# Kernel tuning notes

Hardware: AMD Instinct MI355X
Metric: run time of the kernel (lower is better)

The kernel has to match this reference:

```python
import jax, jax.numpy as jnp
import numpy as np

L, S, N, E, H = 2048, 2048, 4, 1024, 16
D = E // H  # head_dim = 64


def setup_inputs() -> dict:
    key = jax.random.key(0)
    ks = jax.random.split(key, 7)
    scale = 1.0 / np.sqrt(E)
    return {
        "query": jax.random.normal(ks[0], (L, N, E), jnp.float32),
        "key": jax.random.normal(ks[1], (S, N, E), jnp.float32),
        "value": jax.random.normal(ks[2], (S, N, E), jnp.float32),
        "in_proj_w": jax.random.normal(ks[3], (3 * E, E), jnp.float32) * scale,
        "in_proj_b": jax.random.normal(ks[4], (3 * E,), jnp.float32) * 0.01,
        "out_proj_w": jax.random.normal(ks[5], (E, E), jnp.float32) * scale * 0.25,
        "out_proj_b": jax.random.normal(ks[6], (E,), jnp.float32) * 0.01,
    }


def reference(query, key, value, in_proj_w, in_proj_b, out_proj_w, out_proj_b):
    # Split packed in-projection into q/k/v parts (torch layout: [3E, E]).
    wq, wk, wv = in_proj_w[:E], in_proj_w[E:2 * E], in_proj_w[2 * E:]
    bq, bk, bv = in_proj_b[:E], in_proj_b[E:2 * E], in_proj_b[2 * E:]

    def proj(x, w, b):  # (T,N,E) -> (N,H,T,D)
        y = jnp.einsum('tne,fe->tnf', x, w) + b
        T = x.shape[0]
        return y.reshape(T, N, H, D).transpose(1, 2, 0, 3)

    q = proj(query, wq, bq) * (1.0 / np.sqrt(D))  # scale queries
    k = proj(key, wk, bk)
    v = proj(value, wv, bv)

    scores = jnp.einsum('nhld,nhsd->nhls', q, k)  # (N,H,L,S)
    attn = jax.nn.softmax(scores, axis=-1)
    ctx = jnp.einsum('nhls,nhsd->nhld', attn, v)  # (N,H,L,D)
    ctx = ctx.transpose(2, 0, 1, 3).reshape(L, N, E)  # (L,N,E)

    out = jnp.einsum('lne,fe->lnf', ctx, out_proj_w) + out_proj_b
    attn_weights = attn.mean(axis=1)  # (N,L,S), averaged over heads (torch default)
    return out, attn_weights
```

## Files before the change

kernel.cpp:

```cpp
#include <hip/hip_runtime.h>
#include <hip/hip_bf16.h>

#define L_ 2048
#define S_ 2048
#define NB 4
#define E_ 1024
#define H_ 16
#define D_ 64
#define LDT 72
#define NCH (S_ / 64)

typedef __attribute__((ext_vector_type(8))) short bf16x8;
typedef __attribute__((ext_vector_type(4))) float f32x4;

__device__ __forceinline__ short f2bf(float f) {
  union { float f; unsigned u; } v; v.f = f;
  unsigned r = v.u + 0x7FFFu + ((v.u >> 16) & 1u);
  return (short)(r >> 16);
}
__device__ __forceinline__ float bf2f(short s) {
  union { unsigned u; float f; } v; v.u = ((unsigned)(unsigned short)s) << 16;
  return v.f;
}
__device__ __forceinline__ unsigned cvt_pk_bf16(float lo, float hi) {
  unsigned r;
  asm("v_cvt_pk_bf16_f32 %0, %1, %2" : "=v"(r) : "v"(lo), "v"(hi));
  return r;
}

#define LGKM_BARRIER() do {                                   \
    asm volatile("s_waitcnt lgkmcnt(0)" ::: "memory");        \
    __builtin_amdgcn_sched_barrier(0);                        \
    __builtin_amdgcn_s_barrier();                             \
    __builtin_amdgcn_sched_barrier(0);                        \
  } while (0)

__global__ void k_convert(const float* __restrict__ wi, const float* __restrict__ wo,
                          short* __restrict__ wqkv, short* __restrict__ wout) {
  const int n1 = 3 * E_ * E_ / 4;
  const int n2 = E_ * E_ / 4;
  const int stride = gridDim.x * blockDim.x;
  for (int i = blockIdx.x * blockDim.x + threadIdx.x; i < n1 + n2; i += stride) {
    const float4* s; short* d; int j;
    if (i < n1) { s = (const float4*)wi; d = wqkv; j = i; }
    else        { s = (const float4*)wo; d = wout; j = i - n1; }
    float4 v = s[j];
    uint2 o; o.x = cvt_pk_bf16(v.x, v.y); o.y = cvt_pk_bf16(v.z, v.w);
    *(uint2*)&d[(size_t)j * 4] = o;
  }
}

__global__ __launch_bounds__(256) void k_qkv(
    const float* __restrict__ qin, const float* __restrict__ kin, const float* __restrict__ vin,
    const short* __restrict__ wbf, const float* __restrict__ bias,
    short* __restrict__ qh, short* __restrict__ kh, short* __restrict__ vh) {
  __shared__ short As[128 * LDT];
  __shared__ short Bs[128 * LDT];
  const int bm = blockIdx.x;
  const int fbase = blockIdx.y * 128;
  const int mat = fbase >> 10;
  const float* __restrict__ A = (mat == 0) ? qin : (mat == 1) ? kin : vin;
  short* __restrict__ dst = (mat == 0) ? qh : (mat == 1) ? kh : vh;
  const float scale = (mat == 0) ? 0.125f * 1.44269504088896f : 1.0f;
  const int tid = threadIdx.x;
  const int lane = tid & 63, wid = tid >> 6;
  const int wr = wid >> 1, wc = wid & 1;
  const int lr = lane & 15, lk = lane >> 4;
  f32x4 acc[4][4] = {};

  for (int kb = 0; kb < E_; kb += 64) {
#pragma unroll
    for (int i = 0; i < 8; ++i) {
      int f4 = i * 256 + tid;
      int row = f4 >> 4, k4 = f4 & 15;
      float4 v = *(const float4*)&A[(size_t)(bm * 128 + row) * E_ + kb + k4 * 4];
      uint2 o; o.x = cvt_pk_bf16(v.x, v.y); o.y = cvt_pk_bf16(v.z, v.w);
      *(uint2*)&As[row * LDT + k4 * 4] = o;
    }
#pragma unroll
    for (int i = 0; i < 4; ++i) {
      int e8 = i * 256 + tid;
      int row = e8 >> 3, k8 = e8 & 7;
      int4 v = *(const int4*)&wbf[(size_t)(fbase + row) * E_ + kb + k8 * 8];
      *(int4*)&Bs[row * LDT + k8 * 8] = v;
    }
    __syncthreads();
#pragma unroll
    for (int kk = 0; kk < 2; ++kk) {
      bf16x8 a[4], b[4];
#pragma unroll
      for (int fi = 0; fi < 4; ++fi)
        a[fi] = *(const bf16x8*)&As[(wr * 64 + fi * 16 + lr) * LDT + kk * 32 + lk * 8];
#pragma unroll
      for (int ci = 0; ci < 4; ++ci)
        b[ci] = *(const bf16x8*)&Bs[(wc * 64 + ci * 16 + lr) * LDT + kk * 32 + lk * 8];
#pragma unroll
      for (int fi = 0; fi < 4; ++fi)
#pragma unroll
        for (int ci = 0; ci < 4; ++ci)
          acc[fi][ci] = __builtin_amdgcn_mfma_f32_16x16x32_bf16(a[fi], b[ci], acc[fi][ci], 0, 0, 0);
    }
    __syncthreads();
  }
#pragma unroll
  for (int ci = 0; ci < 4; ++ci) {
    const int fg = fbase + wc * 64 + ci * 16 + lr;
    const float b = bias[fg];
    const int col = fg & 1023;
    const int h = col >> 6, d = col & 63;
#pragma unroll
    for (int fi = 0; fi < 4; ++fi)
#pragma unroll
      for (int j = 0; j < 4; ++j) {
        int m = bm * 128 + wr * 64 + fi * 16 + lk * 4 + j;
        int t = m >> 2, n = m & 3;
        float vv = (acc[fi][ci][j] + b) * scale;
        dst[(((size_t)(n * H_ + h) * L_ + t) << 6) + d] = f2bf(vv);
      }
  }
}

__global__ __launch_bounds__(256) void k_vtrans(const short* __restrict__ vh,
                                                short* __restrict__ vt) {
  __shared__ short t[64][LDT];
  const int nh = blockIdx.y;
  const int tb = blockIdx.x;
  const int tid = threadIdx.x;
  const short* __restrict__ src = vh + ((size_t)nh * L_ + tb * 64) * D_;
  short* __restrict__ dst = vt + (size_t)nh * S_ * D_;
#pragma unroll
  for (int i = 0; i < 2; ++i) {
    int v = i * 256 + tid;
    int r = v >> 3, c8 = v & 7;
    *(bf16x8*)&t[r][c8 * 8] = *(const bf16x8*)&src[(size_t)r * D_ + c8 * 8];
  }
  __syncthreads();
#pragma unroll
  for (int i = 0; i < 2; ++i) {
    int v = i * 256 + tid;
    int d = v >> 3, t8 = v & 7;
    bf16x8 o;
#pragma unroll
    for (int e = 0; e < 8; ++e) o[e] = t[t8 * 8 + e][d];
    int sb = tb * 2 + (t8 >> 2);
    *(bf16x8*)&dst[(size_t)sb * (D_ * 32) + d * 32 + (t8 & 3) * 8] = o;
  }
}

__global__ __launch_bounds__(256) void k_stats(
    const short* __restrict__ qh, const short* __restrict__ kh, float* __restrict__ rl) {
  const int nh = blockIdx.y;
  const int qt = blockIdx.x;
  const short* __restrict__ Q = qh + (size_t)nh * L_ * D_;
  const short* __restrict__ K = kh + (size_t)nh * S_ * D_;
  const int tid = threadIdx.x;
  const int lane = tid & 63, wid = tid >> 6;
  const int lr = lane & 15, lk = lane >> 4;
  const int rbase = qt * 128 + wid * 32;
  bf16x8 a[2][2];
#pragma unroll
  for (int ri = 0; ri < 2; ++ri)
#pragma unroll
    for (int kk = 0; kk < 2; ++kk)
      a[ri][kk] = *(const bf16x8*)&Q[(size_t)(rbase + ri * 16 + lr) * D_ + kk * 32 + lk * 8];
  bf16x8 kst[4][2];
#pragma unroll
  for (int ci = 0; ci < 4; ++ci) {
    kst[ci][0] = *(const bf16x8*)&K[(size_t)(ci * 16 + lr) * D_ + lk * 8];
    kst[ci][1] = *(const bf16x8*)&K[(size_t)(ci * 16 + lr) * D_ + 32 + lk * 8];
  }
  float ssum[2][4] = {};
  for (int st = 0; st < S_; st += 64) {
    const int stn = (st + 64 < S_) ? st + 64 : st;
    f32x4 acc[2][4] = {};
#pragma unroll
    for (int ci = 0; ci < 4; ++ci) {
#pragma unroll
      for (int ri = 0; ri < 2; ++ri) {
        acc[ri][ci] = __builtin_amdgcn_mfma_f32_16x16x32_bf16(a[ri][0], kst[ci][0], acc[ri][ci], 0, 0, 0);
        acc[ri][ci] = __builtin_amdgcn_mfma_f32_16x16x32_bf16(a[ri][1], kst[ci][1], acc[ri][ci], 0, 0, 0);
      }
      kst[ci][0] = *(const bf16x8*)&K[(size_t)(stn + ci * 16 + lr) * D_ + lk * 8];
      kst[ci][1] = *(const bf16x8*)&K[(size_t)(stn + ci * 16 + lr) * D_ + 32 + lk * 8];
    }
#pragma unroll
    for (int ri = 0; ri < 2; ++ri)
#pragma unroll
      for (int j = 0; j < 4; ++j) {
        float s = __builtin_amdgcn_exp2f(acc[ri][0][j]) + __builtin_amdgcn_exp2f(acc[ri][1][j]) +
                  __builtin_amdgcn_exp2f(acc[ri][2][j]) + __builtin_amdgcn_exp2f(acc[ri][3][j]);
        s += __shfl_xor(s, 1);
        s += __shfl_xor(s, 2);
        s += __shfl_xor(s, 4);
        s += __shfl_xor(s, 8);
        ssum[ri][j] += s;
      }
  }
  if (lr == 0) {
#pragma unroll
    for (int ri = 0; ri < 2; ++ri)
#pragma unroll
      for (int j = 0; j < 4; ++j)
        rl[(size_t)nh * L_ + rbase + ri * 16 + lk * 4 + j] = 1.0f / ssum[ri][j];
  }
}

__global__ __launch_bounds__(1024) void k_attn(
    const short* __restrict__ qh, const short* __restrict__ kh, const short* __restrict__ vt,
    const float* __restrict__ rl, float* __restrict__ attnw, short* __restrict__ ctx) {
  extern __shared__ char psl[];
  const int bid = blockIdx.x;
  const int xcd = bid & 7;
  const int n = xcd >> 1;
  const int qt = (bid >> 3) | ((xcd & 1) << 5);
  const int tid = threadIdx.x;
  const int h = tid >> 6, lane = tid & 63;
  const int lr = lane & 15, lk = lane >> 4;
  const int rbase = qt * 32;
  const size_t nh = (size_t)(n * H_ + h);
  const short* __restrict__ K = kh + nh * S_ * D_;
  const short* __restrict__ VT = vt + nh * S_ * D_;
  char* const slab0 = psl + h * 4096;

  bf16x8 qf[2][2];
  float rls[2];
  {
    const short* Q = qh + nh * L_ * D_;
#pragma unroll
    for (int li = 0; li < 2; ++li) {
#pragma unroll
      for (int kk = 0; kk < 2; ++kk)
        qf[li][kk] = *(const bf16x8*)&Q[(size_t)(rbase + li * 16 + lr) * D_ + kk * 32 + lk * 8];
      rls[li] = rl[nh * L_ + rbase + li * 16 + lr];
    }
  }
  f32x4 cacc[2][4] = {};
  const int mrow = tid >> 5, mc2 = (tid & 31) * 2;
  float* awp = attnw + ((size_t)n * L_ + rbase + mrow) * S_ + mc2;
  const int moff = mrow * 128 + ((mc2 * 2) ^ ((mrow & 7) << 4));

  for (int ch = 0; ch < NCH; ++ch) {
    const int st = ch * 64;
    char* const sl = slab0 + (ch & 1) * 65536;
    bf16x8 kf[4][2];
#pragma unroll
    for (int u = 0; u < 4; ++u) {
      kf[u][0] = *(const bf16x8*)&K[(size_t)(st + u * 16 + lr) * D_ + lk * 8];
      kf[u][1] = *(const bf16x8*)&K[(size_t)(st + u * 16 + lr) * D_ + 32 + lk * 8];
    }
    bf16x8 vb[4][2];
#pragma unroll
    for (int b = 0; b < 2; ++b) {
      const size_t sb = (size_t)((st >> 5) + b) * (D_ * 32);
#pragma unroll
      for (int ci = 0; ci < 4; ++ci)
        vb[ci][b] = *(const bf16x8*)&VT[sb + (ci * 16 + lr) * 32 + lk * 8];
    }
#pragma unroll
    for (int u = 0; u < 4; ++u) {
#pragma unroll
      for (int li = 0; li < 2; ++li) {
        f32x4 sc = {};
        sc = __builtin_amdgcn_mfma_f32_16x16x32_bf16(kf[u][0], qf[li][0], sc, 0, 0, 0);
        sc = __builtin_amdgcn_mfma_f32_16x16x32_bf16(kf[u][1], qf[li][1], sc, 0, 0, 0);
        uint2 pk;
        pk.x = cvt_pk_bf16(__builtin_amdgcn_exp2f(sc[0]) * rls[li],
                           __builtin_amdgcn_exp2f(sc[1]) * rls[li]);
        pk.y = cvt_pk_bf16(__builtin_amdgcn_exp2f(sc[2]) * rls[li],
                           __builtin_amdgcn_exp2f(sc[3]) * rls[li]);
        const int row = li * 16 + lr;
        *(uint2*)(sl + row * 128 + ((u * 32 + lk * 8) ^ ((row & 7) << 4))) = pk;
      }
    }
#pragma unroll
    for (int b = 0; b < 2; ++b)
#pragma unroll
      for (int li = 0; li < 2; ++li) {
        const int row = li * 16 + lr;
        bf16x8 pa = *(const bf16x8*)(sl + row * 128 + ((b * 64 + lk * 16) ^ ((row & 7) << 4)));
#pragma unroll
        for (int ci = 0; ci < 4; ++ci)
          cacc[li][ci] = __builtin_amdgcn_mfma_f32_16x16x32_bf16(pa, vb[ci][b], cacc[li][ci], 0, 0, 0);
      }
    if (ch > 0) {
      char* const ms = psl + (((ch & 1) ^ 1)) * 65536;
      float s0 = 0.f, s1 = 0.f;
#pragma unroll
      for (int hh = 0; hh < 16; ++hh) {
        short2 m = *(const short2*)(ms + hh * 4096 + moff);
        s0 += bf2f(m.x); s1 += bf2f(m.y);
      }
      *(float2*)&awp[st - 64] = make_float2(s0 * 0.0625f, s1 * 0.0625f);
    }
    LGKM_BARRIER();
  }
  {
    char* const ms = psl + 65536;
    float s0 = 0.f, s1 = 0.f;
#pragma unroll
    for (int hh = 0; hh < 16; ++hh) {
      short2 m = *(const short2*)(ms + hh * 4096 + moff);
      s0 += bf2f(m.x); s1 += bf2f(m.y);
    }
    *(float2*)&awp[S_ - 64] = make_float2(s0 * 0.0625f, s1 * 0.0625f);
  }
#pragma unroll
  for (int li = 0; li < 2; ++li)
#pragma unroll
    for (int ci = 0; ci < 4; ++ci)
#pragma unroll
      for (int j = 0; j < 4; ++j) {
        int row = rbase + li * 16 + lk * 4 + j;
        int d = ci * 16 + lr;
        ctx[((size_t)row * NB + n) * E_ + h * 64 + d] = f2bf(cacc[li][ci][j]);
      }
}

__global__ __launch_bounds__(256) void k_out(
    const short* __restrict__ ctxb, const short* __restrict__ wbf,
    const float* __restrict__ bias, float* __restrict__ out) {
  __shared__ short As[128 * LDT];
  __shared__ short Bs[128 * LDT];
  const int bm = blockIdx.x, bn = blockIdx.y;
  const int tid = threadIdx.x;
  const int lane = tid & 63, wid = tid >> 6;
  const int wr = wid >> 1, wc = wid & 1;
  const int lr = lane & 15, lk = lane >> 4;
  f32x4 acc[4][4] = {};
  for (int kb = 0; kb < E_; kb += 64) {
#pragma unroll
    for (int i = 0; i < 4; ++i) {
      int e8 = i * 256 + tid;
      int row = e8 >> 3, k8 = e8 & 7;
      int4 va = *(const int4*)&ctxb[(size_t)(bm * 128 + row) * E_ + kb + k8 * 8];
      *(int4*)&As[row * LDT + k8 * 8] = va;
      int4 vb = *(const int4*)&wbf[(size_t)(bn * 128 + row) * E_ + kb + k8 * 8];
      *(int4*)&Bs[row * LDT + k8 * 8] = vb;
    }
    __syncthreads();
#pragma unroll
    for (int kk = 0; kk < 2; ++kk) {
      bf16x8 a[4], b[4];
#pragma unroll
      for (int fi = 0; fi < 4; ++fi)
        a[fi] = *(const bf16x8*)&As[(wr * 64 + fi * 16 + lr) * LDT + kk * 32 + lk * 8];
#pragma unroll
      for (int ci = 0; ci < 4; ++ci)
        b[ci] = *(const bf16x8*)&Bs[(wc * 64 + ci * 16 + lr) * LDT + kk * 32 + lk * 8];
#pragma unroll
      for (int fi = 0; fi < 4; ++fi)
#pragma unroll
        for (int ci = 0; ci < 4; ++ci)
          acc[fi][ci] = __builtin_amdgcn_mfma_f32_16x16x32_bf16(a[fi], b[ci], acc[fi][ci], 0, 0, 0);
    }
    __syncthreads();
  }
#pragma unroll
  for (int ci = 0; ci < 4; ++ci) {
    int col = bn * 128 + wc * 64 + ci * 16 + lr;
    float b = bias[col];
#pragma unroll
    for (int fi = 0; fi < 4; ++fi)
#pragma unroll
      for (int j = 0; j < 4; ++j) {
        int m = bm * 128 + wr * 64 + fi * 16 + lk * 4 + j;
        out[(size_t)m * E_ + col] = acc[fi][ci][j] + b;
      }
  }
}

extern "C" void kernel_launch(void* const* d_in, const int* in_sizes, int n_in,
                              void* d_out, int out_size, void* d_ws, size_t ws_size,
                              hipStream_t stream) {
  const float* qin = (const float*)d_in[0];
  const float* kin = (const float*)d_in[1];
  const float* vin = (const float*)d_in[2];
  const float* wi  = (const float*)d_in[3];
  const float* bi  = (const float*)d_in[4];
  const float* wo  = (const float*)d_in[5];
  const float* bo  = (const float*)d_in[6];
  float* out = (float*)d_out;
  float* attnw = out + (size_t)L_ * NB * E_;

  short* wqkv = (short*)d_ws;
  short* wout = wqkv + (size_t)3 * E_ * E_;
  short* qh = wout + (size_t)E_ * E_;
  short* kh = qh + (size_t)NB * L_ * E_;
  short* vh = kh + (size_t)NB * L_ * E_;
  short* vt = vh + (size_t)NB * L_ * E_;
  float* rl = (float*)(vt + (size_t)NB * L_ * E_);
  short* ctx = (short*)(rl + (size_t)NB * H_ * L_);

  k_convert<<<1024, 256, 0, stream>>>(wi, wo, wqkv, wout);
  k_qkv<<<dim3(64, 24), 256, 0, stream>>>(qin, kin, vin, wqkv, bi, qh, kh, vh);
  k_vtrans<<<dim3(32, 64), 256, 0, stream>>>(vh, vt);
  k_stats<<<dim3(16, 64), 256, 0, stream>>>(qh, kh, rl);
  k_attn<<<256, 1024, 131072, stream>>>(qh, kh, vt, rl, attnw, ctx);
  k_out<<<dim3(64, 8), 256, 0, stream>>>(ctx, wout, bo, out);
}
```

Baseline: 453.0 us.

## Split attention over key halves, fuse V transpose into QKV projection

The attention kernel now launches twice as many blocks, and each block handles half of the key chunks. The two partial context results go to separate buffers and are summed in the out-projection load. Shared memory drops to a single 64KB slab, so the double buffering is gone and an extra barrier is added per chunk, which aims for more resident blocks and better CU fill. The separate V-transpose kernel is removed and the QKV projection writes V straight into the transposed layout with scattered 2-byte stores. The partial contexts are rounded to bf16 before they are summed, which adds rounding error, and the ctx traffic doubles.

```diff
diff --git a/kernel.cpp b/kernel.cpp
--- a/kernel.cpp
+++ b/kernel.cpp
@@ -26,6 +26,12 @@
   unsigned r;
   asm("v_cvt_pk_bf16_f32 %0, %1, %2" : "=v"(r) : "v"(lo), "v"(hi));
   return r;
+}
+__device__ __forceinline__ float bfu_lo(unsigned u) {
+  union { unsigned u; float f; } v; v.u = u << 16; return v.f;
+}
+__device__ __forceinline__ float bfu_hi(unsigned u) {
+  union { unsigned u; float f; } v; v.u = u & 0xFFFF0000u; return v.f;
 }
 
 #define LGKM_BARRIER() do {                                   \
@@ -53,14 +59,14 @@
 __global__ __launch_bounds__(256) void k_qkv(
     const float* __restrict__ qin, const float* __restrict__ kin, const float* __restrict__ vin,
     const short* __restrict__ wbf, const float* __restrict__ bias,
-    short* __restrict__ qh, short* __restrict__ kh, short* __restrict__ vh) {
+    short* __restrict__ qh, short* __restrict__ kh, short* __restrict__ vt) {
   __shared__ short As[128 * LDT];
   __shared__ short Bs[128 * LDT];
   const int bm = blockIdx.x;
   const int fbase = blockIdx.y * 128;
   const int mat = fbase >> 10;
   const float* __restrict__ A = (mat == 0) ? qin : (mat == 1) ? kin : vin;
-  short* __restrict__ dst = (mat == 0) ? qh : (mat == 1) ? kh : vh;
+  short* __restrict__ dst = (mat == 0) ? qh : (mat == 1) ? kh : vt;
   const float scale = (mat == 0) ? 0.125f * 1.44269504088896f : 1.0f;
   const int tid = threadIdx.x;
   const int lane = tid & 63, wid = tid >> 6;
@@ -115,35 +121,12 @@
         int m = bm * 128 + wr * 64 + fi * 16 + lk * 4 + j;
         int t = m >> 2, n = m & 3;
         float vv = (acc[fi][ci][j] + b) * scale;
-        dst[(((size_t)(n * H_ + h) * L_ + t) << 6) + d] = f2bf(vv);
-      }
-  }
-}
-
-__global__ __launch_bounds__(256) void k_vtrans(const short* __restrict__ vh,
-                                                short* __restrict__ vt) {
-  __shared__ short t[64][LDT];
-  const int nh = blockIdx.y;
-  const int tb = blockIdx.x;
-  const int tid = threadIdx.x;
-  const short* __restrict__ src = vh + ((size_t)nh * L_ + tb * 64) * D_;
-  short* __restrict__ dst = vt + (size_t)nh * S_ * D_;
-#pragma unroll
-  for (int i = 0; i < 2; ++i) {
-    int v = i * 256 + tid;
-    int r = v >> 3, c8 = v & 7;
-    *(bf16x8*)&t[r][c8 * 8] = *(const bf16x8*)&src[(size_t)r * D_ + c8 * 8];
-  }
-  __syncthreads();
-#pragma unroll
-  for (int i = 0; i < 2; ++i) {
-    int v = i * 256 + tid;
-    int d = v >> 3, t8 = v & 7;
-    bf16x8 o;
-#pragma unroll
-    for (int e = 0; e < 8; ++e) o[e] = t[t8 * 8 + e][d];
-    int sb = tb * 2 + (t8 >> 2);
-    *(bf16x8*)&dst[(size_t)sb * (D_ * 32) + d * 32 + (t8 & 3) * 8] = o;
+        size_t base = (size_t)(n * H_ + h) * (L_ * D_);
+        size_t idx = (mat == 2)
+          ? base + (size_t)(t >> 5) * (D_ * 32) + d * 32 + (t & 31)
+          : base + ((size_t)t << 6) + d;
+        dst[idx] = f2bf(vv);
+      }
   }
 }
 
@@ -205,14 +188,15 @@
   }
 }
 
-__global__ __launch_bounds__(1024) void k_attn(
+__global__ __launch_bounds__(1024, 8) void k_attn(
     const short* __restrict__ qh, const short* __restrict__ kh, const short* __restrict__ vt,
-    const float* __restrict__ rl, float* __restrict__ attnw, short* __restrict__ ctx) {
+    const float* __restrict__ rl, float* __restrict__ attnw, short* __restrict__ ctxp) {
   extern __shared__ char psl[];
   const int bid = blockIdx.x;
   const int xcd = bid & 7;
   const int n = xcd >> 1;
-  const int qt = (bid >> 3) | ((xcd & 1) << 5);
+  const int sh = xcd & 1;
+  const int qt = bid >> 3;
   const int tid = threadIdx.x;
   const int h = tid >> 6, lane = tid & 63;
   const int lr = lane & 15, lk = lane >> 4;
@@ -239,9 +223,9 @@
   float* awp = attnw + ((size_t)n * L_ + rbase + mrow) * S_ + mc2;
   const int moff = mrow * 128 + ((mc2 * 2) ^ ((mrow & 7) << 4));
 
-  for (int ch = 0; ch < NCH; ++ch) {
+  const int ch0 = sh * (NCH / 2), ch1 = ch0 + NCH / 2;
+  for (int ch = ch0; ch < ch1; ++ch) {
     const int st = ch * 64;
-    char* const sl = slab0 + (ch & 1) * 65536;
     bf16x8 kf[4][2];
 #pragma unroll
     for (int u = 0; u < 4; ++u) {
@@ -269,7 +253,7 @@
         pk.y = cvt_pk_bf16(__builtin_amdgcn_exp2f(sc[2]) * rls[li],
                            __builtin_amdgcn_exp2f(sc[3]) * rls[li]);
         const int row = li * 16 + lr;
-        *(uint2*)(sl + row * 128 + ((u * 32 + lk * 8) ^ ((row & 7) << 4))) = pk;
+        *(uint2*)(slab0 + row * 128 + ((u * 32 + lk * 8) ^ ((row & 7) << 4))) = pk;
       }
     }
 #pragma unroll
@@ -277,33 +261,24 @@
 #pragma unroll
       for (int li = 0; li < 2; ++li) {
         const int row = li * 16 + lr;
-        bf16x8 pa = *(const bf16x8*)(sl + row * 128 + ((b * 64 + lk * 16) ^ ((row & 7) << 4)));
+        bf16x8 pa = *(const bf16x8*)(slab0 + row * 128 + ((b * 64 + lk * 16) ^ ((row & 7) << 4)));
 #pragma unroll
         for (int ci = 0; ci < 4; ++ci)
           cacc[li][ci] = __builtin_amdgcn_mfma_f32_16x16x32_bf16(pa, vb[ci][b], cacc[li][ci], 0, 0, 0);
       }
-    if (ch > 0) {
-      char* const ms = psl + (((ch & 1) ^ 1)) * 65536;
+    LGKM_BARRIER();
+    {
       float s0 = 0.f, s1 = 0.f;
 #pragma unroll
       for (int hh = 0; hh < 16; ++hh) {
-        short2 m = *(const short2*)(ms + hh * 4096 + moff);
+        short2 m = *(const short2*)(psl + hh * 4096 + moff);
         s0 += bf2f(m.x); s1 += bf2f(m.y);
       }
-      *(float2*)&awp[st - 64] = make_float2(s0 * 0.0625f, s1 * 0.0625f);
+      *(float2*)&awp[st] = make_float2(s0 * 0.0625f, s1 * 0.0625f);
     }
     LGKM_BARRIER();
   }
-  {
-    char* const ms = psl + 65536;
-    float s0 = 0.f, s1 = 0.f;
-#pragma unroll
-    for (int hh = 0; hh < 16; ++hh) {
-      short2 m = *(const short2*)(ms + hh * 4096 + moff);
-      s0 += bf2f(m.x); s1 += bf2f(m.y);
-    }
-    *(float2*)&awp[S_ - 64] = make_float2(s0 * 0.0625f, s1 * 0.0625f);
-  }
+  short* __restrict__ cp = ctxp + (size_t)sh * (L_ * NB * E_);
 #pragma unroll
   for (int li = 0; li < 2; ++li)
 #pragma unroll
@@ -312,15 +287,17 @@
       for (int j = 0; j < 4; ++j) {
         int row = rbase + li * 16 + lk * 4 + j;
         int d = ci * 16 + lr;
-        ctx[((size_t)row * NB + n) * E_ + h * 64 + d] = f2bf(cacc[li][ci][j]);
+        cp[((size_t)row * NB + n) * E_ + h * 64 + d] = f2bf(cacc[li][ci][j]);
       }
 }
 
 __global__ __launch_bounds__(256) void k_out(
-    const short* __restrict__ ctxb, const short* __restrict__ wbf,
+    const short* __restrict__ ctxp, const short* __restrict__ wbf,
     const float* __restrict__ bias, float* __restrict__ out) {
   __shared__ short As[128 * LDT];
   __shared__ short Bs[128 * LDT];
+  const short* __restrict__ c0 = ctxp;
+  const short* __restrict__ c1 = ctxp + (size_t)(L_ * NB * E_);
   const int bm = blockIdx.x, bn = blockIdx.y;
   const int tid = threadIdx.x;
   const int lane = tid & 63, wid = tid >> 6;
@@ -332,8 +309,15 @@
     for (int i = 0; i < 4; ++i) {
       int e8 = i * 256 + tid;
       int row = e8 >> 3, k8 = e8 & 7;
-      int4 va = *(const int4*)&ctxb[(size_t)(bm * 128 + row) * E_ + kb + k8 * 8];
-      *(int4*)&As[row * LDT + k8 * 8] = va;
+      size_t idx = (size_t)(bm * 128 + row) * E_ + kb + k8 * 8;
+      uint4 va = *(const uint4*)&c0[idx];
+      uint4 vc = *(const uint4*)&c1[idx];
+      uint4 r;
+      r.x = cvt_pk_bf16(bfu_lo(va.x) + bfu_lo(vc.x), bfu_hi(va.x) + bfu_hi(vc.x));
+      r.y = cvt_pk_bf16(bfu_lo(va.y) + bfu_lo(vc.y), bfu_hi(va.y) + bfu_hi(vc.y));
+      r.z = cvt_pk_bf16(bfu_lo(va.z) + bfu_lo(vc.z), bfu_hi(va.z) + bfu_hi(vc.z));
+      r.w = cvt_pk_bf16(bfu_lo(va.w) + bfu_lo(vc.w), bfu_hi(va.w) + bfu_hi(vc.w));
+      *(uint4*)&As[row * LDT + k8 * 8] = r;
       int4 vb = *(const int4*)&wbf[(size_t)(bn * 128 + row) * E_ + kb + k8 * 8];
       *(int4*)&Bs[row * LDT + k8 * 8] = vb;
     }
@@ -386,15 +370,13 @@
   short* wout = wqkv + (size_t)3 * E_ * E_;
   short* qh = wout + (size_t)E_ * E_;
   short* kh = qh + (size_t)NB * L_ * E_;
-  short* vh = kh + (size_t)NB * L_ * E_;
-  short* vt = vh + (size_t)NB * L_ * E_;
+  short* vt = kh + (size_t)NB * L_ * E_;
   float* rl = (float*)(vt + (size_t)NB * L_ * E_);
-  short* ctx = (short*)(rl + (size_t)NB * H_ * L_);
+  short* ctxp = (short*)(rl + (size_t)NB * H_ * L_);
 
   k_convert<<<1024, 256, 0, stream>>>(wi, wo, wqkv, wout);
-  k_qkv<<<dim3(64, 24), 256, 0, stream>>>(qin, kin, vin, wqkv, bi, qh, kh, vh);
-  k_vtrans<<<dim3(32, 64), 256, 0, stream>>>(vh, vt);
+  k_qkv<<<dim3(64, 24), 256, 0, stream>>>(qin, kin, vin, wqkv, bi, qh, kh, vt);
   k_stats<<<dim3(16, 64), 256, 0, stream>>>(qh, kh, rl);
-  k_attn<<<256, 1024, 131072, stream>>>(qh, kh, vt, rl, attnw, ctx);
-  k_out<<<dim3(64, 8), 256, 0, stream>>>(ctx, wout, bo, out);
-}
+  k_attn<<<512, 1024, 65536, stream>>>(qh, kh, vt, rl, attnw, ctxp);
+  k_out<<<dim3(64, 8), 256, 0, stream>>>(ctxp, wout, bo, out);
+}
```

After: 800.0 us. 1.77x slower.
